# Performance work log

Hardware: AMD Instinct MI355X
Metric: run time of the kernel (lower is better)

Reference implementation:

```python
import jax, jax.numpy as jnp
import numpy as np

C = 256
C8 = C // 8


def setup_inputs() -> dict:
    key = jax.random.key(0)
    ks = jax.random.split(key, 9)
    B, H, W = 4, 64, 64
    s = 1.0 / np.sqrt(C)
    return {
        "pre_feat": jax.random.normal(ks[0], (B, C, H, W), jnp.float32),
        "post_feat": jax.random.normal(ks[1], (B, C, H, W), jnp.float32),
        "Wq": jax.random.normal(ks[2], (C8, C), jnp.float32) * s,
        "bq": jnp.zeros((C8,), jnp.float32),
        "Wk": jax.random.normal(ks[3], (C8, C), jnp.float32) * s,
        "bk": jnp.zeros((C8,), jnp.float32),
        "Wv": jax.random.normal(ks[4], (C, C), jnp.float32) * s,
        "bv": jnp.zeros((C,), jnp.float32),
        "gamma": jnp.zeros((1,), jnp.float32),
    }


def reference(pre_feat, post_feat, Wq, bq, Wk, bk, Wv, bv, gamma):
    B, Cc, H, W = pre_feat.shape
    N = H * W
    pre = pre_feat.reshape(B, Cc, N)    # (B, C, N)
    post = post_feat.reshape(B, Cc, N)
    # 1x1 convs == per-pixel linear projections
    q = jnp.einsum('dc,bcn->bdn', Wq, post) + bq[None, :, None]  # (B, C8, N)
    k = jnp.einsum('dc,bcn->bdn', Wk, pre) + bk[None, :, None]   # (B, C8, N)
    v = jnp.einsum('dc,bcn->bdn', Wv, pre) + bv[None, :, None]   # (B, C, N)
    # energy[b,i,j] = <q[b,:,i], k[b,:,j]>  (unscaled)
    energy = jnp.einsum('bdi,bdj->bij', q, k)                    # (B, N, N)
    attention = jax.nn.softmax(energy, axis=-1)
    # out[b,c,i] = sum_j v[b,c,j] * attention[b,i,j]
    out = jnp.einsum('bcj,bij->bci', v, attention).reshape(B, Cc, H, W)
    return gamma[0] * out + post_feat
```

## Files before the change

### kernel.cpp

```cpp
#include <hip/hip_runtime.h>
#include <hip/hip_bf16.h>

#define Bn 4
#define Cn 256
#define Dn 32
#define Nn 4096

typedef __bf16 bf16x8 __attribute__((ext_vector_type(8)));
typedef short shortx4 __attribute__((ext_vector_type(4)));
typedef float f32x4 __attribute__((ext_vector_type(4)));

__device__ __forceinline__ float bf2f(unsigned short u) {
  unsigned int v = ((unsigned int)u) << 16;
  return __builtin_bit_cast(float, v);
}
__device__ __forceinline__ unsigned short f2bf(float f) {
  unsigned int v = __builtin_bit_cast(unsigned int, f);
  v += 0x7FFFu + ((v >> 16) & 1u);
  return (unsigned short)(v >> 16);
}
__device__ __forceinline__ unsigned int pk2(float a, float b) {
  union { __hip_bfloat162 h; unsigned int u; } x;
  x.h = __float22bfloat162_rn(make_float2(a, b));
  return x.u;
}
__device__ __forceinline__ bf16x8 ldfrag(const unsigned short* p) {
  return __builtin_bit_cast(bf16x8, *(const uint4*)p);
}
__device__ __forceinline__ uint4 pack8(const float* p) {
  float4 a = *(const float4*)p;
  float4 b = *(const float4*)(p + 4);
  union { unsigned int u2[4]; uint4 u; } x;
  x.u2[0] = pk2(a.x, a.y); x.u2[1] = pk2(a.z, a.w);
  x.u2[2] = pk2(b.x, b.y); x.u2[3] = pk2(b.z, b.w);
  return x.u;
}
__device__ __forceinline__ void async16(unsigned short* lds, const unsigned short* g) {
  __builtin_amdgcn_global_load_lds(
      (const __attribute__((address_space(1))) unsigned int*)g,
      (__attribute__((address_space(3))) unsigned int*)lds, 16, 0, 0);
}

__global__ __launch_bounds__(256) void prep(
    const float* __restrict__ pre, const float* __restrict__ post,
    const float* __restrict__ Wq, const float* __restrict__ Wk,
    const float* __restrict__ Wv,
    unsigned short* __restrict__ preT, unsigned short* __restrict__ postT,
    unsigned short* __restrict__ preBf, unsigned short* __restrict__ WqBf,
    unsigned short* __restrict__ WkBf, unsigned short* __restrict__ WvBf)
{
  if (blockIdx.x >= 1024) {
    int idx8 = ((blockIdx.x - 1024) * 256 + threadIdx.x) * 8;
    if (idx8 < 8192) {
      *(uint4*)(WqBf + idx8) = pack8(Wq + idx8);
    } else if (idx8 < 16384) {
      *(uint4*)(WkBf + idx8 - 8192) = pack8(Wk + idx8 - 8192);
    } else {
      *(uint4*)(WvBf + idx8 - 16384) = pack8(Wv + idx8 - 16384);
    }
    return;
  }
  __shared__ __align__(16) unsigned short sA[64][72];
  __shared__ __align__(16) unsigned short sB[64][72];
  const int tid = threadIdx.x;
  const int b = blockIdx.x >> 8;
  const int c0 = ((blockIdx.x >> 6) & 3) << 6;
  const int i0 = (blockIdx.x & 63) << 6;
  const int r = tid >> 2, ch = (tid & 3) << 4;

  const float* pPost = post + ((size_t)b * Cn + c0 + r) * Nn + i0 + ch;
  const float* pPre  = pre  + ((size_t)b * Cn + c0 + r) * Nn + i0 + ch;
  *(uint4*)&sA[r][ch]     = pack8(pPost);
  *(uint4*)&sA[r][ch + 8] = pack8(pPost + 8);
  uint4 pb0 = pack8(pPre), pb1 = pack8(pPre + 8);
  *(uint4*)&sB[r][ch]     = pb0;
  *(uint4*)&sB[r][ch + 8] = pb1;
  __syncthreads();

#pragma unroll
  for (int e = 0; e < 2; e++) {
    int h = ((tid & 3) << 1) + e;
    int g = (h >> 2) << 5, q = (h & 3) << 2;
    union { unsigned short s[8]; uint4 u; } o;
    *(uint2*)&o.s[0] = *(const uint2*)&sB[r][g + q];
    *(uint2*)&o.s[4] = *(const uint2*)&sB[r][g + 16 + q];
    *(uint4*)(preBf + ((size_t)b * Cn + c0 + r) * Nn + i0 + h * 8) = o.u;
  }
  union { unsigned short s[16]; uint4 u[2]; } tp, tk;
#pragma unroll
  for (int e = 0; e < 16; e++) {
    tp.s[e] = sA[ch + e][r];
    tk.s[e] = sB[ch + e][r];
  }
  const size_t trow = ((size_t)b * Nn + i0 + r) * Cn + c0 + ch;
  *(uint4*)(postT + trow) = tp.u[0];
  *(uint4*)(postT + trow + 8) = tp.u[1];
  *(uint4*)(preT + trow) = tk.u[0];
  *(uint4*)(preT + trow + 8) = tk.u[1];
}

__global__ __launch_bounds__(256) void qk_proj(
    const unsigned short* __restrict__ preT, const unsigned short* __restrict__ postT,
    const unsigned short* __restrict__ WqBf, const float* __restrict__ bq,
    const unsigned short* __restrict__ WkBf, const float* __restrict__ bk,
    unsigned short* __restrict__ Qt, unsigned short* __restrict__ Kt)
{
  const int tid = threadIdx.x;
  const int lane = tid & 63, w = tid >> 6;
  const int quad = lane >> 4, n16 = lane & 15;
  const int b = blockIdx.x >> 7;
  const int i0 = (blockIdx.x & 127) << 5;
  const int isub = w & 1, dh = w >> 1;
  const int i = i0 + isub * 16 + n16;
  const size_t rowB = ((size_t)b * Nn + i) * Cn;

  const f32x4 zz = {0.f, 0.f, 0.f, 0.f};
  f32x4 aq = zz, ak = zz;
#pragma unroll
  for (int kc = 0; kc < 8; kc++) {
    bf16x8 bfq = ldfrag(postT + rowB + kc * 32 + quad * 8);
    bf16x8 bfk = ldfrag(preT + rowB + kc * 32 + quad * 8);
    bf16x8 awq = ldfrag(WqBf + (size_t)(dh * 16 + n16) * Cn + kc * 32 + quad * 8);
    bf16x8 awk = ldfrag(WkBf + (size_t)(dh * 16 + n16) * Cn + kc * 32 + quad * 8);
    aq = __builtin_amdgcn_mfma_f32_16x16x32_bf16(awq, bfq, aq, 0, 0, 0);
    ak = __builtin_amdgcn_mfma_f32_16x16x32_bf16(awk, bfk, ak, 0, 0, 0);
  }
  const float LOG2E = 1.44269504f;
  union { unsigned short s[4]; uint2 u; } oq, ok;
#pragma unroll
  for (int r = 0; r < 4; r++) {
    int d = dh * 16 + quad * 4 + r;
    oq.s[r] = f2bf((aq[r] + bq[d]) * LOG2E);
    ok.s[r] = f2bf(ak[r] + bk[d]);
  }
  *(uint2*)(Qt + ((size_t)b * Nn + i) * Dn + dh * 16 + quad * 4) = oq.u;
  *(uint2*)(Kt + ((size_t)b * Nn + i) * Dn + dh * 16 + quad * 4) = ok.u;
}

__global__ __launch_bounds__(128, 2) void flash_attn(
    const unsigned short* __restrict__ Qt, const unsigned short* __restrict__ Kt,
    const unsigned short* __restrict__ preBf,
    unsigned short* __restrict__ Opart, float* __restrict__ Lpart)
{
  __shared__ __align__(16) unsigned short sX[256 * 64];

  const int tid = threadIdx.x;
  const int lane = tid & 63, w = tid >> 6;
  const int quad = lane >> 4, n16 = lane & 15;
  const int b = blockIdx.x >> 8;
  const int js = (blockIdx.x >> 6) & 3;
  const int it = blockIdx.x & 63;
  const int iw = it * 64 + w * 32;
  const int jbase = js * 1024;

  bf16x8 qf[2];
#pragma unroll
  for (int sub = 0; sub < 2; sub++)
    qf[sub] = ldfrag(Qt + ((size_t)b * Nn + iw + sub * 16 + n16) * Dn + quad * 8);

  const f32x4 zz = {0.f, 0.f, 0.f, 0.f};
  f32x4 acc[2][16];
#pragma unroll
  for (int sub = 0; sub < 2; sub++)
#pragma unroll
    for (int ct = 0; ct < 16; ct++) acc[sub][ct] = zz;
  float lrow[2] = {0.f, 0.f};

  const int lrw = lane >> 3;
  const size_t laneoff = (size_t)lrw * Nn + (size_t)(((lane & 7) ^ lrw) << 3);
  const unsigned short* preB = preBf + (size_t)b * Cn * Nn + laneoff;
  const int xsw = n16 & 7;
  const int xoff0 = (quad ^ xsw) << 3;
  const int xoff1 = ((4 + quad) ^ xsw) << 3;

  auto stage = [&](int j0) {
#pragma unroll
    for (int k = 0; k < 16; k++) {
      const int rb = (k * 2 + w) * 8;
      async16(sX + rb * 64 + (lane << 3), preB + (size_t)rb * Nn + j0);
    }
  };
  auto loadK = [&](int j0, bf16x8 kf[4]) {
#pragma unroll
    for (int jt = 0; jt < 4; jt++)
      kf[jt] = ldfrag(Kt + ((size_t)b * Nn + j0 + jt * 16 + n16) * Dn + quad * 8);
  };
  auto makeP = [&](const bf16x8 kf[4], shortx4 pbDst[2][4]) {
    f32x4 sc[2][4];
#pragma unroll
    for (int jt = 0; jt < 4; jt++) {
      sc[0][jt] = __builtin_amdgcn_mfma_f32_16x16x32_bf16(kf[jt], qf[0], zz, 0, 0, 0);
      sc[1][jt] = __builtin_amdgcn_mfma_f32_16x16x32_bf16(kf[jt], qf[1], zz, 0, 0, 0);
    }
#pragma unroll
    for (int sub = 0; sub < 2; sub++) {
      float ps = 0.f;
#pragma unroll
      for (int jt = 0; jt < 4; jt++) {
        float p0 = exp2f(fminf(sc[sub][jt][0], 101.f));
        float p1 = exp2f(fminf(sc[sub][jt][1], 101.f));
        float p2 = exp2f(fminf(sc[sub][jt][2], 101.f));
        float p3 = exp2f(fminf(sc[sub][jt][3], 101.f));
        ps += (p0 + p1) + (p2 + p3);
        union { unsigned int u2[2]; shortx4 v; } u;
        u.u2[0] = pk2(p0, p1);
        u.u2[1] = pk2(p2, p3);
        pbDst[sub][jt] = u.v;
      }
      ps += __shfl_xor(ps, 16);
      ps += __shfl_xor(ps, 32);
      lrow[sub] += ps;
    }
  };

  stage(jbase);
  shortx4 pb[2][4];
  {
    bf16x8 kf0[4];
    loadK(jbase, kf0);
    makeP(kf0, pb);
  }
  __syncthreads();

  for (int t = 0; t < 16; ++t) {
    const int jn = jbase + (t + 1) * 64;
    bf16x8 kfn[4];
    if (t < 15) loadK(jn, kfn);

#pragma unroll
    for (int jt2 = 0; jt2 < 2; jt2++) {
      const int xoff = jt2 ? xoff1 : xoff0;
#pragma unroll
      for (int ct = 0; ct < 16; ct++) {
        union { bf16x8 v; shortx4 h[2]; } av;
        av.v = ldfrag(&sX[(ct * 16 + n16) * 64 + xoff]);
        acc[0][ct] = __builtin_amdgcn_mfma_f32_16x16x16bf16_1k(av.h[0], pb[0][jt2 * 2], acc[0][ct], 0, 0, 0);
        acc[0][ct] = __builtin_amdgcn_mfma_f32_16x16x16bf16_1k(av.h[1], pb[0][jt2 * 2 + 1], acc[0][ct], 0, 0, 0);
        acc[1][ct] = __builtin_amdgcn_mfma_f32_16x16x16bf16_1k(av.h[0], pb[1][jt2 * 2], acc[1][ct], 0, 0, 0);
        acc[1][ct] = __builtin_amdgcn_mfma_f32_16x16x16bf16_1k(av.h[1], pb[1][jt2 * 2 + 1], acc[1][ct], 0, 0, 0);
      }
    }
    __syncthreads();
    if (t < 15) {
      stage(jn);
      shortx4 pbn[2][4];
      makeP(kfn, pbn);
#pragma unroll
      for (int sub = 0; sub < 2; sub++)
#pragma unroll
        for (int jt = 0; jt < 4; jt++) pb[sub][jt] = pbn[sub][jt];
    }
    __syncthreads();
  }

  const size_t base = (size_t)(js * 4 + b) * Nn;
#pragma unroll
  for (int sub = 0; sub < 2; sub++) {
    const int i = iw + sub * 16 + n16;
    if (quad == 0) Lpart[base + i] = lrow[sub];
#pragma unroll
    for (int ct = 0; ct < 16; ct++) {
      union { unsigned int u2[2]; uint2 u; } pk;
      pk.u2[0] = pk2(acc[sub][ct][0], acc[sub][ct][1]);
      pk.u2[1] = pk2(acc[sub][ct][2], acc[sub][ct][3]);
      *(uint2*)(Opart + (base + i) * 256 + ct * 16 + quad * 4) = pk.u;
    }
  }
}

__global__ __launch_bounds__(256) void combine(
    const unsigned short* __restrict__ Opart, const float* __restrict__ Lpart,
    const unsigned short* __restrict__ WvBf, const float* __restrict__ bv,
    const float* __restrict__ post, const float* __restrict__ gamma,
    float* __restrict__ out)
{
  __shared__ __align__(16) unsigned short sU[32 * 264];
  __shared__ float sL[32];

  const int tid = threadIdx.x;
  const int lane = tid & 63, w = tid >> 6;
  const int quad = lane >> 4, n16 = lane & 15;
  const int b = blockIdx.x >> 7;
  const int i0 = (blockIdx.x & 127) << 5;

  if (tid < 32) {
    float l = 0.f;
#pragma unroll
    for (int js = 0; js < 4; js++) l += Lpart[(size_t)(js * 4 + b) * Nn + i0 + tid];
    sL[tid] = 1.f / l;
  }
  __syncthreads();

  const int il = tid >> 3, cbase = (tid & 7) << 5;
  const float inv = sL[il];
#pragma unroll
  for (int u4 = 0; u4 < 4; u4++) {
    const int c8 = cbase + u4 * 8;
    float a[8] = {0.f, 0.f, 0.f, 0.f, 0.f, 0.f, 0.f, 0.f};
#pragma unroll
    for (int js = 0; js < 4; js++) {
      uint4 uu = *(const uint4*)(Opart + ((size_t)(js * 4 + b) * Nn + i0 + il) * 256 + c8);
      const unsigned short* us = (const unsigned short*)&uu;
#pragma unroll
      for (int e = 0; e < 8; e++) a[e] += bf2f(us[e]);
    }
    union { unsigned int u2[4]; uint4 u; } pk;
#pragma unroll
    for (int e2 = 0; e2 < 4; e2++) pk.u2[e2] = pk2(a[2 * e2] * inv, a[2 * e2 + 1] * inv);
    *(uint4*)&sU[il * 264 + c8] = pk.u;
  }
  __syncthreads();

  bf16x8 ub[2][8];
#pragma unroll
  for (int sub = 0; sub < 2; sub++)
#pragma unroll
    for (int kc = 0; kc < 8; kc++)
      ub[sub][kc] = ldfrag(&sU[(sub * 16 + n16) * 264 + kc * 32 + quad * 8]);

  const float g = gamma[0];
  const f32x4 zz = {0.f, 0.f, 0.f, 0.f};
#pragma unroll
  for (int e = 0; e < 4; e++) {
    const int ct2 = w * 4 + e;
    f32x4 o0 = zz, o1 = zz;
#pragma unroll
    for (int kc = 0; kc < 8; kc++) {
      bf16x8 awv = ldfrag(WvBf + (size_t)(ct2 * 16 + n16) * Cn + kc * 32 + quad * 8);
      o0 = __builtin_amdgcn_mfma_f32_16x16x32_bf16(awv, ub[0][kc], o0, 0, 0, 0);
      o1 = __builtin_amdgcn_mfma_f32_16x16x32_bf16(awv, ub[1][kc], o1, 0, 0, 0);
    }
#pragma unroll
    for (int r = 0; r < 4; r++) {
      const int c = ct2 * 16 + quad * 4 + r;
      const float bb = bv[c];
      size_t a0 = ((size_t)b * Cn + c) * Nn + i0 + n16;
      out[a0] = g * (o0[r] + bb) + post[a0];
      out[a0 + 16] = g * (o1[r] + bb) + post[a0 + 16];
    }
  }
}

extern "C" void kernel_launch(void* const* d_in, const int* in_sizes, int n_in,
                              void* d_out, int out_size, void* d_ws, size_t ws_size,
                              hipStream_t stream) {
  const float* pre   = (const float*)d_in[0];
  const float* post  = (const float*)d_in[1];
  const float* Wq    = (const float*)d_in[2];
  const float* bq    = (const float*)d_in[3];
  const float* Wk    = (const float*)d_in[4];
  const float* bk    = (const float*)d_in[5];
  const float* Wv    = (const float*)d_in[6];
  const float* bv    = (const float*)d_in[7];
  const float* gamma = (const float*)d_in[8];
  float* out = (float*)d_out;

  unsigned short* ws = (unsigned short*)d_ws;
  unsigned short* Qt    = ws;
  unsigned short* Kt    = Qt + (size_t)Bn * Nn * Dn;
  unsigned short* preBf = Kt + (size_t)Bn * Nn * Dn;
  unsigned short* WqBf  = preBf + (size_t)Bn * Cn * Nn;
  unsigned short* WkBf  = WqBf + Dn * Cn;
  unsigned short* WvBf  = WkBf + Dn * Cn;
  float* Lpart = (float*)(WvBf + Cn * Cn);
  unsigned short* Opart = (unsigned short*)(Lpart + 4 * Bn * Nn);
  unsigned short* preT  = Opart;
  unsigned short* postT = Opart + (size_t)Bn * Nn * Cn;

  prep<<<1064, 256, 0, stream>>>(pre, post, Wq, Wk, Wv,
                                 preT, postT, preBf, WqBf, WkBf, WvBf);
  qk_proj<<<512, 256, 0, stream>>>(preT, postT, WqBf, bq, WkBf, bk, Qt, Kt);
  flash_attn<<<1024, 128, 0, stream>>>(Qt, Kt, preBf, Opart, Lpart);
  combine<<<512, 256, 0, stream>>>(Opart, Lpart, WvBf, bv, post, gamma, out);
}
```

Baseline: 202.7 us.

## Fuse prep with QK projection, double-buffer flash V tiles via LDS P

Merges the prep and qk_proj kernels so Q/K projections read fp32 inputs directly with strided loads, dropping the transposed bf16 copies and one launch. It also stops reordering the pre tensor into a swizzled bf16 layout. The flash kernel now double-buffers the V tile in LDS and shares the probability tile through LDS so each wave covers half the channels for all 64 rows, using wider MFMA. The combine kernel uses 16-row blocks for more parallelism. Risks include uncoalesced strided fp32 loads in the projection, higher LDS usage lowering occupancy, and a possible mismatch between the new linear preBf layout and the swizzled reads in the flash kernel.

```diff
diff --git a/kernel.cpp b/kernel.cpp
--- a/kernel.cpp
+++ b/kernel.cpp
@@ -7,7 +7,6 @@
 #define Nn 4096
 
 typedef __bf16 bf16x8 __attribute__((ext_vector_type(8)));
-typedef short shortx4 __attribute__((ext_vector_type(4)));
 typedef float f32x4 __attribute__((ext_vector_type(4)));
 
 __device__ __forceinline__ float bf2f(unsigned short u) {
@@ -35,95 +34,72 @@
   x.u2[2] = pk2(b.x, b.y); x.u2[3] = pk2(b.z, b.w);
   return x.u;
 }
+__device__ __forceinline__ bf16x8 ldfrag_f32(const float* p) {
+  float4 a = *(const float4*)p;
+  float4 b = *(const float4*)(p + 4);
+  union { unsigned int u2[4]; bf16x8 v; } x;
+  x.u2[0] = pk2(a.x, a.y); x.u2[1] = pk2(a.z, a.w);
+  x.u2[2] = pk2(b.x, b.y); x.u2[3] = pk2(b.z, b.w);
+  return x.v;
+}
 __device__ __forceinline__ void async16(unsigned short* lds, const unsigned short* g) {
   __builtin_amdgcn_global_load_lds(
       (const __attribute__((address_space(1))) unsigned int*)g,
       (__attribute__((address_space(3))) unsigned int*)lds, 16, 0, 0);
 }
 
-__global__ __launch_bounds__(256) void prep(
+__global__ __launch_bounds__(256) void qkprep(
     const float* __restrict__ pre, const float* __restrict__ post,
-    const float* __restrict__ Wq, const float* __restrict__ Wk,
+    const float* __restrict__ Wq, const float* __restrict__ bq,
+    const float* __restrict__ Wk, const float* __restrict__ bk,
     const float* __restrict__ Wv,
-    unsigned short* __restrict__ preT, unsigned short* __restrict__ postT,
-    unsigned short* __restrict__ preBf, unsigned short* __restrict__ WqBf,
-    unsigned short* __restrict__ WkBf, unsigned short* __restrict__ WvBf)
+    unsigned short* __restrict__ Qt, unsigned short* __restrict__ Kt,
+    unsigned short* __restrict__ preBf, unsigned short* __restrict__ WvBf)
 {
-  if (blockIdx.x >= 1024) {
-    int idx8 = ((blockIdx.x - 1024) * 256 + threadIdx.x) * 8;
-    if (idx8 < 8192) {
-      *(uint4*)(WqBf + idx8) = pack8(Wq + idx8);
-    } else if (idx8 < 16384) {
-      *(uint4*)(WkBf + idx8 - 8192) = pack8(Wk + idx8 - 8192);
+  const int blk = blockIdx.x, tid = threadIdx.x;
+  if (blk >= 512) {
+    if (blk < 1024) {
+      size_t base = ((size_t)(blk - 512) * 256 + tid) * 32;
+#pragma unroll
+      for (int u = 0; u < 4; u++)
+        *(uint4*)(preBf + base + u * 8) = pack8(pre + base + u * 8);
     } else {
-      *(uint4*)(WvBf + idx8 - 16384) = pack8(Wv + idx8 - 16384);
+      size_t base = ((size_t)(blk - 1024) * 256 + tid) * 32;
+#pragma unroll
+      for (int u = 0; u < 4; u++)
+        *(uint4*)(WvBf + base + u * 8) = pack8(Wv + base + u * 8);
     }
     return;
   }
-  __shared__ __align__(16) unsigned short sA[64][72];
-  __shared__ __align__(16) unsigned short sB[64][72];
-  const int tid = threadIdx.x;
-  const int b = blockIdx.x >> 8;
-  const int c0 = ((blockIdx.x >> 6) & 3) << 6;
-  const int i0 = (blockIdx.x & 63) << 6;
-  const int r = tid >> 2, ch = (tid & 3) << 4;
-
-  const float* pPost = post + ((size_t)b * Cn + c0 + r) * Nn + i0 + ch;
-  const float* pPre  = pre  + ((size_t)b * Cn + c0 + r) * Nn + i0 + ch;
-  *(uint4*)&sA[r][ch]     = pack8(pPost);
-  *(uint4*)&sA[r][ch + 8] = pack8(pPost + 8);
-  uint4 pb0 = pack8(pPre), pb1 = pack8(pPre + 8);
-  *(uint4*)&sB[r][ch]     = pb0;
-  *(uint4*)&sB[r][ch + 8] = pb1;
-  __syncthreads();
-
-#pragma unroll
-  for (int e = 0; e < 2; e++) {
-    int h = ((tid & 3) << 1) + e;
-    int g = (h >> 2) << 5, q = (h & 3) << 2;
-    union { unsigned short s[8]; uint4 u; } o;
-    *(uint2*)&o.s[0] = *(const uint2*)&sB[r][g + q];
-    *(uint2*)&o.s[4] = *(const uint2*)&sB[r][g + 16 + q];
-    *(uint4*)(preBf + ((size_t)b * Cn + c0 + r) * Nn + i0 + h * 8) = o.u;
-  }
-  union { unsigned short s[16]; uint4 u[2]; } tp, tk;
-#pragma unroll
-  for (int e = 0; e < 16; e++) {
-    tp.s[e] = sA[ch + e][r];
-    tk.s[e] = sB[ch + e][r];
-  }
-  const size_t trow = ((size_t)b * Nn + i0 + r) * Cn + c0 + ch;
-  *(uint4*)(postT + trow) = tp.u[0];
-  *(uint4*)(postT + trow + 8) = tp.u[1];
-  *(uint4*)(preT + trow) = tk.u[0];
-  *(uint4*)(preT + trow + 8) = tk.u[1];
-}
-
-__global__ __launch_bounds__(256) void qk_proj(
-    const unsigned short* __restrict__ preT, const unsigned short* __restrict__ postT,
-    const unsigned short* __restrict__ WqBf, const float* __restrict__ bq,
-    const unsigned short* __restrict__ WkBf, const float* __restrict__ bk,
-    unsigned short* __restrict__ Qt, unsigned short* __restrict__ Kt)
-{
-  const int tid = threadIdx.x;
   const int lane = tid & 63, w = tid >> 6;
   const int quad = lane >> 4, n16 = lane & 15;
-  const int b = blockIdx.x >> 7;
-  const int i0 = (blockIdx.x & 127) << 5;
+  const int b = blk >> 7;
+  const int i0 = (blk & 127) << 5;
   const int isub = w & 1, dh = w >> 1;
   const int i = i0 + isub * 16 + n16;
-  const size_t rowB = ((size_t)b * Nn + i) * Cn;
 
   const f32x4 zz = {0.f, 0.f, 0.f, 0.f};
   f32x4 aq = zz, ak = zz;
+  const float* postB = post + (size_t)b * Cn * Nn + i;
+  const float* preB  = pre  + (size_t)b * Cn * Nn + i;
+
 #pragma unroll
   for (int kc = 0; kc < 8; kc++) {
-    bf16x8 bfq = ldfrag(postT + rowB + kc * 32 + quad * 8);
-    bf16x8 bfk = ldfrag(preT + rowB + kc * 32 + quad * 8);
-    bf16x8 awq = ldfrag(WqBf + (size_t)(dh * 16 + n16) * Cn + kc * 32 + quad * 8);
-    bf16x8 awk = ldfrag(WkBf + (size_t)(dh * 16 + n16) * Cn + kc * 32 + quad * 8);
-    aq = __builtin_amdgcn_mfma_f32_16x16x32_bf16(awq, bfq, aq, 0, 0, 0);
-    ak = __builtin_amdgcn_mfma_f32_16x16x32_bf16(awk, bfk, ak, 0, 0, 0);
+    const int c0 = kc * 32 + quad * 8;
+    const float* pp = postB + (size_t)c0 * Nn;
+    const float* pr = preB + (size_t)c0 * Nn;
+    union { unsigned int u2[4]; bf16x8 v; } bp, bq8;
+#pragma unroll
+    for (int e2 = 0; e2 < 4; e2++) {
+      float p0 = pp[(size_t)(2 * e2) * Nn], p1 = pp[(size_t)(2 * e2 + 1) * Nn];
+      float r0 = pr[(size_t)(2 * e2) * Nn], r1 = pr[(size_t)(2 * e2 + 1) * Nn];
+      bp.u2[e2] = pk2(p0, p1);
+      bq8.u2[e2] = pk2(r0, r1);
+    }
+    bf16x8 awq = ldfrag_f32(Wq + (size_t)(dh * 16 + n16) * Cn + kc * 32 + quad * 8);
+    bf16x8 awk = ldfrag_f32(Wk + (size_t)(dh * 16 + n16) * Cn + kc * 32 + quad * 8);
+    aq = __builtin_amdgcn_mfma_f32_16x16x32_bf16(awq, bp.v, aq, 0, 0, 0);
+    ak = __builtin_amdgcn_mfma_f32_16x16x32_bf16(awk, bq8.v, ak, 0, 0, 0);
   }
   const float LOG2E = 1.44269504f;
   union { unsigned short s[4]; uint2 u; } oq, ok;
@@ -142,7 +118,8 @@
     const unsigned short* __restrict__ preBf,
     unsigned short* __restrict__ Opart, float* __restrict__ Lpart)
 {
-  __shared__ __align__(16) unsigned short sX[256 * 64];
+  __shared__ __align__(16) unsigned short sX[2][256 * 64];
+  __shared__ __align__(16) unsigned short Pl[64][72];
 
   const int tid = threadIdx.x;
   const int lane = tid & 63, w = tid >> 6;
@@ -150,34 +127,33 @@
   const int b = blockIdx.x >> 8;
   const int js = (blockIdx.x >> 6) & 3;
   const int it = blockIdx.x & 63;
-  const int iw = it * 64 + w * 32;
+  const int i0 = it * 64;
   const int jbase = js * 1024;
 
   bf16x8 qf[2];
 #pragma unroll
-  for (int sub = 0; sub < 2; sub++)
-    qf[sub] = ldfrag(Qt + ((size_t)b * Nn + iw + sub * 16 + n16) * Dn + quad * 8);
+  for (int s2 = 0; s2 < 2; s2++)
+    qf[s2] = ldfrag(Qt + ((size_t)b * Nn + i0 + (w * 2 + s2) * 16 + n16) * Dn + quad * 8);
 
   const f32x4 zz = {0.f, 0.f, 0.f, 0.f};
-  f32x4 acc[2][16];
-#pragma unroll
-  for (int sub = 0; sub < 2; sub++)
-#pragma unroll
-    for (int ct = 0; ct < 16; ct++) acc[sub][ct] = zz;
+  f32x4 acc[4][8];
+#pragma unroll
+  for (int sub = 0; sub < 4; sub++)
+#pragma unroll
+    for (int ct = 0; ct < 8; ct++) acc[sub][ct] = zz;
   float lrow[2] = {0.f, 0.f};
 
-  const int lrw = lane >> 3;
-  const size_t laneoff = (size_t)lrw * Nn + (size_t)(((lane & 7) ^ lrw) << 3);
+  const size_t laneoff = (size_t)(lane >> 3) * Nn + (size_t)(((lane & 7) ^ (lane >> 3)) << 3);
   const unsigned short* preB = preBf + (size_t)b * Cn * Nn + laneoff;
   const int xsw = n16 & 7;
   const int xoff0 = (quad ^ xsw) << 3;
   const int xoff1 = ((4 + quad) ^ xsw) << 3;
 
-  auto stage = [&](int j0) {
+  auto stage = [&](int j0, int buf) {
 #pragma unroll
     for (int k = 0; k < 16; k++) {
       const int rb = (k * 2 + w) * 8;
-      async16(sX + rb * 64 + (lane << 3), preB + (size_t)rb * Nn + j0);
+      async16(&sX[buf][rb * 64] + (lane << 3), preB + (size_t)rb * Nn + j0);
     }
   };
   auto loadK = [&](int j0, bf16x8 kf[4]) {
@@ -185,7 +161,7 @@
     for (int jt = 0; jt < 4; jt++)
       kf[jt] = ldfrag(Kt + ((size_t)b * Nn + j0 + jt * 16 + n16) * Dn + quad * 8);
   };
-  auto makeP = [&](const bf16x8 kf[4], shortx4 pbDst[2][4]) {
+  auto makeP = [&](const bf16x8 kf[4]) {
     f32x4 sc[2][4];
 #pragma unroll
     for (int jt = 0; jt < 4; jt++) {
@@ -193,77 +169,78 @@
       sc[1][jt] = __builtin_amdgcn_mfma_f32_16x16x32_bf16(kf[jt], qf[1], zz, 0, 0, 0);
     }
 #pragma unroll
-    for (int sub = 0; sub < 2; sub++) {
+    for (int s2 = 0; s2 < 2; s2++) {
+      const int irow = w * 32 + s2 * 16 + n16;
       float ps = 0.f;
 #pragma unroll
       for (int jt = 0; jt < 4; jt++) {
-        float p0 = exp2f(fminf(sc[sub][jt][0], 101.f));
-        float p1 = exp2f(fminf(sc[sub][jt][1], 101.f));
-        float p2 = exp2f(fminf(sc[sub][jt][2], 101.f));
-        float p3 = exp2f(fminf(sc[sub][jt][3], 101.f));
+        float p0 = exp2f(fminf(sc[s2][jt][0], 101.f));
+        float p1 = exp2f(fminf(sc[s2][jt][1], 101.f));
+        float p2 = exp2f(fminf(sc[s2][jt][2], 101.f));
+        float p3 = exp2f(fminf(sc[s2][jt][3], 101.f));
         ps += (p0 + p1) + (p2 + p3);
-        union { unsigned int u2[2]; shortx4 v; } u;
-        u.u2[0] = pk2(p0, p1);
-        u.u2[1] = pk2(p2, p3);
-        pbDst[sub][jt] = u.v;
+        union { unsigned int u2[2]; uint2 u; } pk;
+        pk.u2[0] = pk2(p0, p1);
+        pk.u2[1] = pk2(p2, p3);
+        *(uint2*)&Pl[irow][jt * 16 + quad * 4] = pk.u;
       }
       ps += __shfl_xor(ps, 16);
       ps += __shfl_xor(ps, 32);
-      lrow[sub] += ps;
+      lrow[s2] += ps;
     }
   };
 
-  stage(jbase);
-  shortx4 pb[2][4];
-  {
-    bf16x8 kf0[4];
-    loadK(jbase, kf0);
-    makeP(kf0, pb);
-  }
+  bf16x8 kf[4];
+  stage(jbase, 0);
+  loadK(jbase, kf);
+  makeP(kf);
+  loadK(jbase + 64, kf);
   __syncthreads();
 
   for (int t = 0; t < 16; ++t) {
-    const int jn = jbase + (t + 1) * 64;
-    bf16x8 kfn[4];
-    if (t < 15) loadK(jn, kfn);
-
-#pragma unroll
-    for (int jt2 = 0; jt2 < 2; jt2++) {
-      const int xoff = jt2 ? xoff1 : xoff0;
-#pragma unroll
-      for (int ct = 0; ct < 16; ct++) {
-        union { bf16x8 v; shortx4 h[2]; } av;
-        av.v = ldfrag(&sX[(ct * 16 + n16) * 64 + xoff]);
-        acc[0][ct] = __builtin_amdgcn_mfma_f32_16x16x16bf16_1k(av.h[0], pb[0][jt2 * 2], acc[0][ct], 0, 0, 0);
-        acc[0][ct] = __builtin_amdgcn_mfma_f32_16x16x16bf16_1k(av.h[1], pb[0][jt2 * 2 + 1], acc[0][ct], 0, 0, 0);
-        acc[1][ct] = __builtin_amdgcn_mfma_f32_16x16x16bf16_1k(av.h[0], pb[1][jt2 * 2], acc[1][ct], 0, 0, 0);
-        acc[1][ct] = __builtin_amdgcn_mfma_f32_16x16x16bf16_1k(av.h[1], pb[1][jt2 * 2 + 1], acc[1][ct], 0, 0, 0);
+    const unsigned short* sXc = sX[t & 1];
+    if (t < 15) stage(jbase + (t + 1) * 64, (t + 1) & 1);
+
+#pragma unroll
+    for (int kc = 0; kc < 2; kc++) {
+      const int xo = kc ? xoff1 : xoff0;
+      bf16x8 pB[4];
+#pragma unroll
+      for (int sub = 0; sub < 4; sub++)
+        pB[sub] = ldfrag(&Pl[sub * 16 + n16][kc * 32 + quad * 8]);
+#pragma unroll
+      for (int ct = 0; ct < 8; ct++) {
+        const int crow = w * 128 + ct * 16 + n16;
+        bf16x8 av = ldfrag(&sXc[crow * 64 + xo]);
+        acc[0][ct] = __builtin_amdgcn_mfma_f32_16x16x32_bf16(av, pB[0], acc[0][ct], 0, 0, 0);
+        acc[1][ct] = __builtin_amdgcn_mfma_f32_16x16x32_bf16(av, pB[1], acc[1][ct], 0, 0, 0);
+        acc[2][ct] = __builtin_amdgcn_mfma_f32_16x16x32_bf16(av, pB[2], acc[2][ct], 0, 0, 0);
+        acc[3][ct] = __builtin_amdgcn_mfma_f32_16x16x32_bf16(av, pB[3], acc[3][ct], 0, 0, 0);
       }
     }
     __syncthreads();
     if (t < 15) {
-      stage(jn);
-      shortx4 pbn[2][4];
-      makeP(kfn, pbn);
-#pragma unroll
-      for (int sub = 0; sub < 2; sub++)
-#pragma unroll
-        for (int jt = 0; jt < 4; jt++) pb[sub][jt] = pbn[sub][jt];
+      makeP(kf);
+      const int tn = (t + 2 < 16) ? (t + 2) : 15;
+      loadK(jbase + tn * 64, kf);
     }
     __syncthreads();
   }
 
   const size_t base = (size_t)(js * 4 + b) * Nn;
-#pragma unroll
-  for (int sub = 0; sub < 2; sub++) {
-    const int i = iw + sub * 16 + n16;
-    if (quad == 0) Lpart[base + i] = lrow[sub];
-#pragma unroll
-    for (int ct = 0; ct < 16; ct++) {
+  if (quad == 0) {
+    Lpart[base + i0 + w * 32 + n16] = lrow[0];
+    Lpart[base + i0 + w * 32 + 16 + n16] = lrow[1];
+  }
+#pragma unroll
+  for (int sub = 0; sub < 4; sub++) {
+    const int i = i0 + sub * 16 + n16;
+#pragma unroll
+    for (int ct = 0; ct < 8; ct++) {
       union { unsigned int u2[2]; uint2 u; } pk;
       pk.u2[0] = pk2(acc[sub][ct][0], acc[sub][ct][1]);
       pk.u2[1] = pk2(acc[sub][ct][2], acc[sub][ct][3]);
-      *(uint2*)(Opart + (base + i) * 256 + ct * 16 + quad * 4) = pk.u;
+      *(uint2*)(Opart + (base + i) * 256 + w * 128 + ct * 16 + quad * 4) = pk.u;
     }
   }
 }
@@ -274,16 +251,16 @@
     const float* __restrict__ post, const float* __restrict__ gamma,
     float* __restrict__ out)
 {
-  __shared__ __align__(16) unsigned short sU[32 * 264];
-  __shared__ float sL[32];
+  __shared__ __align__(16) unsigned short sU[16 * 264];
+  __shared__ float sL[16];
 
   const int tid = threadIdx.x;
   const int lane = tid & 63, w = tid >> 6;
   const int quad = lane >> 4, n16 = lane & 15;
-  const int b = blockIdx.x >> 7;
-  const int i0 = (blockIdx.x & 127) << 5;
-
-  if (tid < 32) {
+  const int b = blockIdx.x >> 8;
+  const int i0 = (blockIdx.x & 255) << 4;
+
+  if (tid < 16) {
     float l = 0.f;
 #pragma unroll
     for (int js = 0; js < 4; js++) l += Lpart[(size_t)(js * 4 + b) * Nn + i0 + tid];
@@ -291,11 +268,11 @@
   }
   __syncthreads();
 
-  const int il = tid >> 3, cbase = (tid & 7) << 5;
-  const float inv = sL[il];
-#pragma unroll
-  for (int u4 = 0; u4 < 4; u4++) {
-    const int c8 = cbase + u4 * 8;
+#pragma unroll
+  for (int pass = 0; pass < 2; pass++) {
+    const int s = tid + pass * 256;
+    const int il = s >> 5, c8 = (s & 31) << 3;
+    const float inv = sL[il];
     float a[8] = {0.f, 0.f, 0.f, 0.f, 0.f, 0.f, 0.f, 0.f};
 #pragma unroll
     for (int js = 0; js < 4; js++) {
@@ -311,32 +288,27 @@
   }
   __syncthreads();
 
-  bf16x8 ub[2][8];
-#pragma unroll
-  for (int sub = 0; sub < 2; sub++)
-#pragma unroll
-    for (int kc = 0; kc < 8; kc++)
-      ub[sub][kc] = ldfrag(&sU[(sub * 16 + n16) * 264 + kc * 32 + quad * 8]);
+  bf16x8 ub[8];
+#pragma unroll
+  for (int kc = 0; kc < 8; kc++)
+    ub[kc] = ldfrag(&sU[n16 * 264 + kc * 32 + quad * 8]);
 
   const float g = gamma[0];
   const f32x4 zz = {0.f, 0.f, 0.f, 0.f};
 #pragma unroll
   for (int e = 0; e < 4; e++) {
     const int ct2 = w * 4 + e;
-    f32x4 o0 = zz, o1 = zz;
+    f32x4 o = zz;
 #pragma unroll
     for (int kc = 0; kc < 8; kc++) {
       bf16x8 awv = ldfrag(WvBf + (size_t)(ct2 * 16 + n16) * Cn + kc * 32 + quad * 8);
-      o0 = __builtin_amdgcn_mfma_f32_16x16x32_bf16(awv, ub[0][kc], o0, 0, 0, 0);
-      o1 = __builtin_amdgcn_mfma_f32_16x16x32_bf16(awv, ub[1][kc], o1, 0, 0, 0);
+      o = __builtin_amdgcn_mfma_f32_16x16x32_bf16(awv, ub[kc], o, 0, 0, 0);
     }
 #pragma unroll
     for (int r = 0; r < 4; r++) {
       const int c = ct2 * 16 + quad * 4 + r;
-      const float bb = bv[c];
-      size_t a0 = ((size_t)b * Cn + c) * Nn + i0 + n16;
-      out[a0] = g * (o0[r] + bb) + post[a0];
-      out[a0 + 16] = g * (o1[r] + bb) + post[a0 + 16];
+      const size_t addr = ((size_t)b * Cn + c) * Nn + i0 + n16;
+      out[addr] = g * (o[r] + bv[c]) + post[addr];
     }
   }
 }
@@ -359,17 +331,12 @@
   unsigned short* Qt    = ws;
   unsigned short* Kt    = Qt + (size_t)Bn * Nn * Dn;
   unsigned short* preBf = Kt + (size_t)Bn * Nn * Dn;
-  unsigned short* WqBf  = preBf + (size_t)Bn * Cn * Nn;
-  unsigned short* WkBf  = WqBf + Dn * Cn;
-  unsigned short* WvBf  = WkBf + Dn * Cn;
+  unsigned short* WvBf  = preBf + (size_t)Bn * Cn * Nn;
   float* Lpart = (float*)(WvBf + Cn * Cn);
   unsigned short* Opart = (unsigned short*)(Lpart + 4 * Bn * Nn);
-  unsigned short* preT  = Opart;
-  unsigned short* postT = Opart + (size_t)Bn * Nn * Cn;
-
-  prep<<<1064, 256, 0, stream>>>(pre, post, Wq, Wk, Wv,
-                                 preT, postT, preBf, WqBf, WkBf, WvBf);
-  qk_proj<<<512, 256, 0, stream>>>(preT, postT, WqBf, bq, WkBf, bk, Qt, Kt);
+
+  qkprep<<<1032, 256, 0, stream>>>(pre, post, Wq, bq, Wk, bk, Wv,
+                                   Qt, Kt, preBf, WvBf);
   flash_attn<<<1024, 128, 0, stream>>>(Qt, Kt, preBf, Opart, Lpart);
-  combine<<<512, 256, 0, stream>>>(Opart, Lpart, WvBf, bv, post, gamma, out);
-}
+  combine<<<1024, 256, 0, stream>>>(Opart, Lpart, WvBf, bv, post, gamma, out);
+}
```

Result: slower. 228.4 us (+12.7%).
